# Performance work log

Measured on AMD Instinct MI355X. Metric: run time of the kernel, lower is better.

The kernel has to match this reference:

```python
import jax, jax.numpy as jnp
import numpy as np


def setup_inputs() -> dict:
    key = jax.random.key(0)
    k1, k2, k3 = jax.random.split(key, 3)
    B, N, E, A = 1024, 64, 64, 32
    emb_inputs = jax.random.normal(k1, (B, N, E), dtype=jnp.float32)
    W1 = jax.random.normal(k2, (E, A), dtype=jnp.float32) * (1.0 / np.sqrt(E))
    b1 = jnp.zeros((A,), dtype=jnp.float32)
    W2 = jax.random.normal(k3, (A, 1), dtype=jnp.float32) * (1.0 / np.sqrt(A))
    b2 = jnp.zeros((1,), dtype=jnp.float32)
    return {"emb_inputs": emb_inputs, "W1": W1, "b1": b1, "W2": W2, "b2": b2,
            "num_fields": N}


def reference(emb_inputs, W1, b1, W2, b2, num_fields):
    # Pairwise interaction indices (i < j), same order as torch double loop
    rowidx, colidx = np.triu_indices(num_fields, k=1)
    rowidx = jnp.asarray(rowidx)
    colidx = jnp.asarray(colidx)
    # inner: (B, NC2, E) elementwise product of field pairs
    inner = emb_inputs[:, rowidx] * emb_inputs[:, colidx]
    # tiny attention MLP: E -> A -> 1, softmax over the pair dim
    h = jax.nn.relu(jnp.einsum('bpe,ea->bpa', inner, W1) + b1)
    logits = jnp.einsum('bpa,ao->bpo', h, W2) + b2          # (B, NC2, 1)
    attn_scores = jax.nn.softmax(logits, axis=1)            # (B, NC2, 1)
    # dropout layers are identity in eval mode
    outputs = jnp.sum(inner * attn_scores, axis=1)          # (B, E)
    return outputs, attn_scores
```

## Files before the change

kernel.cpp:

```cpp
#include <hip/hip_runtime.h>

#define BATCH   1024
#define NF      64
#define EDIM    64
#define ADIM    32
#define NPAIR   2016
#define NTILE   126
#define XSTR    72

typedef _Float16 f16;
typedef f16   f16x4 __attribute__((ext_vector_type(4)));
typedef f16   f16x8 __attribute__((ext_vector_type(8)));
typedef float f32x4 __attribute__((ext_vector_type(4)));

__global__ __launch_bounds__(256) void afm_kernel(
    const float* __restrict__ emb,
    const float* __restrict__ W1,
    const float* __restrict__ b1,
    const float* __restrict__ W2,
    const float* __restrict__ b2,
    float* __restrict__ out_vec,
    float* __restrict__ out_attn)
{
    __shared__ __align__(16) f16 xs[NF * XSTR];
    __shared__ __align__(16) f16 Xt[EDIM * XSTR];
    __shared__ __align__(16) f16 As[NF * XSTR];
    __shared__ float logits[NPAIR];
    __shared__ unsigned short pairIJ[NPAIR];
    __shared__ float red[8];
    __shared__ float partial[4][EDIM];

    const int t    = threadIdx.x;
    const int b    = blockIdx.x;
    const int wid  = t >> 6;
    const int lane = t & 63;
    const int g    = lane >> 4;
    const int m16  = lane & 15;

    const float4* xg4 = (const float4*)(emb + (size_t)b * NF * EDIM);
    #pragma unroll
    for (int it = 0; it < 4; ++it) {
        int idx = t + it * 256;
        int f = idx >> 4, e4 = (idx & 15) * 4;
        float4 v = xg4[idx];
        f16 h0 = (f16)v.x, h1 = (f16)v.y, h2 = (f16)v.z, h3 = (f16)v.w;
        f16x4 pk = {h0, h1, h2, h3};
        *(f16x4*)&xs[f * XSTR + e4] = pk;
        Xt[(e4 + 0) * XSTR + f] = h0;
        Xt[(e4 + 1) * XSTR + f] = h1;
        Xt[(e4 + 2) * XSTR + f] = h2;
        Xt[(e4 + 3) * XSTR + f] = h3;
    }

    for (int p = t; p < NPAIR; p += 256) {
        int i = (int)(63.5f - 0.5f * sqrtf(16129.0f - 8.0f * (float)p));
        int Ti = (i * (127 - i)) >> 1;
        if (p < Ti)      { --i; Ti = (i * (127 - i)) >> 1; }
        else { int Tn = ((i + 1) * (126 - i)) >> 1; if (p >= Tn) { ++i; Ti = Tn; } }
        int j = p - Ti + i + 1;
        pairIJ[p] = (unsigned short)((i << 8) | j);
    }

    f16x8 w1f[2][2];
    #pragma unroll
    for (int kh = 0; kh < 2; ++kh)
        #pragma unroll
        for (int nh = 0; nh < 2; ++nh)
            #pragma unroll
            for (int j = 0; j < 8; ++j)
                w1f[kh][nh][j] =
                    (f16)W1[(kh * 32 + 8 * g + j) * ADIM + nh * 16 + m16];

    float b1v[2][4], w2v[2][4];
    #pragma unroll
    for (int nh = 0; nh < 2; ++nh)
        #pragma unroll
        for (int r = 0; r < 4; ++r) {
            b1v[nh][r] = b1[nh * 16 + 4 * g + r];
            w2v[nh][r] = W2[nh * 16 + 4 * g + r];
        }
    const float b2s = b2[0];
    __syncthreads();

    for (int tile = wid; tile < NTILE; tile += 4) {
        const int p  = tile * 16 + m16;
        const int ij = pairIJ[p];
        const f16* xi = &xs[(ij >> 8) * XSTR];
        const f16* xj = &xs[(ij & 255) * XSTR];

        f16x8 xi0 = *(const f16x8*)(xi + 8 * g);
        f16x8 xi1 = *(const f16x8*)(xi + 32 + 8 * g);
        f16x8 xj0 = *(const f16x8*)(xj + 8 * g);
        f16x8 xj1 = *(const f16x8*)(xj + 32 + 8 * g);
        f16x8 bi0 = xi0 * xj0;
        f16x8 bi1 = xi1 * xj1;

        f32x4 acc0 = {0.f, 0.f, 0.f, 0.f};
        f32x4 acc1 = {0.f, 0.f, 0.f, 0.f};
        acc0 = __builtin_amdgcn_mfma_f32_16x16x32_f16(w1f[0][0], bi0, acc0, 0, 0, 0);
        acc1 = __builtin_amdgcn_mfma_f32_16x16x32_f16(w1f[0][1], bi0, acc1, 0, 0, 0);
        acc0 = __builtin_amdgcn_mfma_f32_16x16x32_f16(w1f[1][0], bi1, acc0, 0, 0, 0);
        acc1 = __builtin_amdgcn_mfma_f32_16x16x32_f16(w1f[1][1], bi1, acc1, 0, 0, 0);

        float tr = 0.f;
        #pragma unroll
        for (int r = 0; r < 4; ++r) {
            tr += fmaxf(acc0[r] + b1v[0][r], 0.f) * w2v[0][r];
            tr += fmaxf(acc1[r] + b1v[1][r], 0.f) * w2v[1][r];
        }
        tr += __shfl_xor(tr, 16);
        tr += __shfl_xor(tr, 32);
        if (g == 0) logits[p] = tr + b2s;
    }
    __syncthreads();

    float lv[8];
    #pragma unroll
    for (int k = 0; k < 8; ++k) {
        int p = t + 256 * k;
        lv[k] = (p < NPAIR) ? logits[p] : -INFINITY;
    }
    float m = lv[0];
    #pragma unroll
    for (int k = 1; k < 8; ++k) m = fmaxf(m, lv[k]);
    #pragma unroll
    for (int off = 32; off; off >>= 1) m = fmaxf(m, __shfl_xor(m, off));
    if (lane == 0) red[wid] = m;
    __syncthreads();
    if (t == 0) red[4] = fmaxf(fmaxf(red[0], red[1]), fmaxf(red[2], red[3]));
    __syncthreads();
    m = red[4];

    float s = 0.0f;
    #pragma unroll
    for (int k = 0; k < 8; ++k) {
        float ev = __expf(lv[k] - m);
        lv[k] = ev;
        s += ev;
    }
    #pragma unroll
    for (int off = 32; off; off >>= 1) s += __shfl_xor(s, off);
    __syncthreads();
    if (lane == 0) red[wid] = s;
    __syncthreads();
    if (t == 0) red[5] = red[0] + red[1] + red[2] + red[3];
    __syncthreads();
    const float inv = 1.0f / red[5];

    #pragma unroll
    for (int k = 0; k < 8; ++k) {
        int p = t + 256 * k;
        if (p < NPAIR) {
            float av = lv[k] * inv;
            out_attn[(size_t)b * NPAIR + p] = av;
            f16 ah = (f16)av;
            int ij = pairIJ[p];
            int i = ij >> 8, j = ij & 255;
            As[i * XSTR + j] = ah;
            As[j * XSTR + i] = ah;
        }
    }
    if (t < NF) As[t * XSTR + t] = (f16)0.f;
    __syncthreads();

    const int itile = wid;
    f32x4 yacc[4];
    #pragma unroll
    for (int et = 0; et < 4; ++et) yacc[et] = (f32x4){0.f, 0.f, 0.f, 0.f};

    const f16* arow = &As[(itile * 16 + m16) * XSTR];
    f16x8 af0 = *(const f16x8*)(arow + 8 * g);
    f16x8 af1 = *(const f16x8*)(arow + 32 + 8 * g);
    #pragma unroll
    for (int et = 0; et < 4; ++et) {
        const f16* xtr = &Xt[(et * 16 + m16) * XSTR];
        f16x8 bf0 = *(const f16x8*)(xtr + 8 * g);
        f16x8 bf1 = *(const f16x8*)(xtr + 32 + 8 * g);
        yacc[et] = __builtin_amdgcn_mfma_f32_16x16x32_f16(af0, bf0, yacc[et], 0, 0, 0);
        yacc[et] = __builtin_amdgcn_mfma_f32_16x16x32_f16(af1, bf1, yacc[et], 0, 0, 0);
    }

    #pragma unroll
    for (int et = 0; et < 4; ++et) {
        float v = 0.f;
        #pragma unroll
        for (int r = 0; r < 4; ++r) {
            int i = itile * 16 + 4 * g + r;
            int e = et * 16 + m16;
            v = fmaf((float)xs[i * XSTR + e], yacc[et][r], v);
        }
        v += __shfl_xor(v, 16);
        v += __shfl_xor(v, 32);
        if (g == 0) partial[wid][et * 16 + m16] = v;
    }
    __syncthreads();
    if (t < EDIM)
        out_vec[(size_t)b * EDIM + t] = 0.5f *
            (partial[0][t] + partial[1][t] + partial[2][t] + partial[3][t]);
}

extern "C" void kernel_launch(void* const* d_in, const int* in_sizes, int n_in,
                              void* d_out, int out_size, void* d_ws, size_t ws_size,
                              hipStream_t stream) {
    const float* emb = (const float*)d_in[0];
    const float* W1  = (const float*)d_in[1];
    const float* b1  = (const float*)d_in[2];
    const float* W2  = (const float*)d_in[3];
    const float* b2  = (const float*)d_in[4];
    float* out_vec  = (float*)d_out;
    float* out_attn = (float*)d_out + (size_t)BATCH * EDIM;

    afm_kernel<<<BATCH, 256, 0, stream>>>(emb, W1, b1, W2, b2, out_vec, out_attn);
}
```

Measured before the change: 28.93 us.

## Rework pair scoring with 32x32 MFMA tiles and DPP-rotated field operands

Replaces the per-pair lookup table and 16x16 MFMA tiles with a structured schedule. Each wave keeps 32 row-field vectors in registers and rotates column-field vectors across lanes with DPP, then scores pairs through 32x32x16 MFMAs. The pair index is computed analytically. The transposed X copy is now built by a separate packed pass, and launch bounds request 4 blocks per SM. This aims to cut LDS traffic and the index table overhead, but adds DPP shuffles, register pressure and a runtime probe of the DPP rotation direction.

```diff
diff --git a/kernel.cpp b/kernel.cpp
--- a/kernel.cpp
+++ b/kernel.cpp
@@ -5,15 +5,19 @@
 #define EDIM    64
 #define ADIM    32
 #define NPAIR   2016
-#define NTILE   126
 #define XSTR    72
 
 typedef _Float16 f16;
-typedef f16   f16x4 __attribute__((ext_vector_type(4)));
-typedef f16   f16x8 __attribute__((ext_vector_type(8)));
-typedef float f32x4 __attribute__((ext_vector_type(4)));
-
-__global__ __launch_bounds__(256) void afm_kernel(
+typedef f16   f16x4  __attribute__((ext_vector_type(4)));
+typedef f16   f16x8  __attribute__((ext_vector_type(8)));
+typedef float f32x4  __attribute__((ext_vector_type(4)));
+typedef float f32x16 __attribute__((ext_vector_type(16)));
+
+__device__ __forceinline__ f16x8 asH(int4 v) {
+    union { int4 i; f16x8 h; } u; u.i = v; return u.h;
+}
+
+__global__ __launch_bounds__(256, 4) void afm_kernel(
     const float* __restrict__ emb,
     const float* __restrict__ W1,
     const float* __restrict__ b1,
@@ -26,7 +30,6 @@
     __shared__ __align__(16) f16 Xt[EDIM * XSTR];
     __shared__ __align__(16) f16 As[NF * XSTR];
     __shared__ float logits[NPAIR];
-    __shared__ unsigned short pairIJ[NPAIR];
     __shared__ float red[8];
     __shared__ float partial[4][EDIM];
 
@@ -36,6 +39,10 @@
     const int lane = t & 63;
     const int g    = lane >> 4;
     const int m16  = lane & 15;
+    const int h    = lane >> 5;
+    const int l32  = lane & 31;
+    const int l16  = lane & 15;
+    const int hb   = l32 >> 4;
 
     const float4* xg4 = (const float4*)(emb + (size_t)b * NF * EDIM);
     #pragma unroll
@@ -43,74 +50,136 @@
         int idx = t + it * 256;
         int f = idx >> 4, e4 = (idx & 15) * 4;
         float4 v = xg4[idx];
-        f16 h0 = (f16)v.x, h1 = (f16)v.y, h2 = (f16)v.z, h3 = (f16)v.w;
-        f16x4 pk = {h0, h1, h2, h3};
+        f16x4 pk = {(f16)v.x, (f16)v.y, (f16)v.z, (f16)v.w};
         *(f16x4*)&xs[f * XSTR + e4] = pk;
-        Xt[(e4 + 0) * XSTR + f] = h0;
-        Xt[(e4 + 1) * XSTR + f] = h1;
-        Xt[(e4 + 2) * XSTR + f] = h2;
-        Xt[(e4 + 3) * XSTR + f] = h3;
-    }
-
-    for (int p = t; p < NPAIR; p += 256) {
-        int i = (int)(63.5f - 0.5f * sqrtf(16129.0f - 8.0f * (float)p));
-        int Ti = (i * (127 - i)) >> 1;
-        if (p < Ti)      { --i; Ti = (i * (127 - i)) >> 1; }
-        else { int Tn = ((i + 1) * (126 - i)) >> 1; if (p >= Tn) { ++i; Ti = Tn; } }
-        int j = p - Ti + i + 1;
-        pairIJ[p] = (unsigned short)((i << 8) | j);
-    }
-
-    f16x8 w1f[2][2];
-    #pragma unroll
-    for (int kh = 0; kh < 2; ++kh)
-        #pragma unroll
-        for (int nh = 0; nh < 2; ++nh)
+    }
+
+    f16x8 w1a[4];
+    #pragma unroll
+    for (int q = 0; q < 4; ++q)
+        #pragma unroll
+        for (int jj = 0; jj < 8; ++jj)
+            w1a[q][jj] = (f16)W1[(16 * q + 8 * h + jj) * ADIM + l32];
+
+    float b1v[16], w2v[16];
+    #pragma unroll
+    for (int r = 0; r < 16; ++r) {
+        int a = (r & 3) + 8 * (r >> 2) + 4 * h;
+        b1v[r] = b1[a];
+        w2v[r] = W2[a];
+    }
+    const float b2s = b2[0];
+    __syncthreads();
+
+    {
+        const unsigned short* xsu = (const unsigned short*)xs;
+        #pragma unroll
+        for (int it = 0; it < 2; ++it) {
+            int cid = t + it * 256;
+            int e = cid & 63, c = cid >> 6;
+            unsigned int d[4];
             #pragma unroll
-            for (int j = 0; j < 8; ++j)
-                w1f[kh][nh][j] =
-                    (f16)W1[(kh * 32 + 8 * g + j) * ADIM + nh * 16 + m16];
-
-    float b1v[2][4], w2v[2][4];
-    #pragma unroll
-    for (int nh = 0; nh < 2; ++nh)
-        #pragma unroll
-        for (int r = 0; r < 4; ++r) {
-            b1v[nh][r] = b1[nh * 16 + 4 * g + r];
-            w2v[nh][r] = W2[nh * 16 + 4 * g + r];
-        }
-    const float b2s = b2[0];
-    __syncthreads();
-
-    for (int tile = wid; tile < NTILE; tile += 4) {
-        const int p  = tile * 16 + m16;
-        const int ij = pairIJ[p];
-        const f16* xi = &xs[(ij >> 8) * XSTR];
-        const f16* xj = &xs[(ij & 255) * XSTR];
-
-        f16x8 xi0 = *(const f16x8*)(xi + 8 * g);
-        f16x8 xi1 = *(const f16x8*)(xi + 32 + 8 * g);
-        f16x8 xj0 = *(const f16x8*)(xj + 8 * g);
-        f16x8 xj1 = *(const f16x8*)(xj + 32 + 8 * g);
-        f16x8 bi0 = xi0 * xj0;
-        f16x8 bi1 = xi1 * xj1;
-
-        f32x4 acc0 = {0.f, 0.f, 0.f, 0.f};
-        f32x4 acc1 = {0.f, 0.f, 0.f, 0.f};
-        acc0 = __builtin_amdgcn_mfma_f32_16x16x32_f16(w1f[0][0], bi0, acc0, 0, 0, 0);
-        acc1 = __builtin_amdgcn_mfma_f32_16x16x32_f16(w1f[0][1], bi0, acc1, 0, 0, 0);
-        acc0 = __builtin_amdgcn_mfma_f32_16x16x32_f16(w1f[1][0], bi1, acc0, 0, 0, 0);
-        acc1 = __builtin_amdgcn_mfma_f32_16x16x32_f16(w1f[1][1], bi1, acc1, 0, 0, 0);
-
-        float tr = 0.f;
-        #pragma unroll
-        for (int r = 0; r < 4; ++r) {
-            tr += fmaxf(acc0[r] + b1v[0][r], 0.f) * w2v[0][r];
-            tr += fmaxf(acc1[r] + b1v[1][r], 0.f) * w2v[1][r];
-        }
-        tr += __shfl_xor(tr, 16);
+            for (int r2 = 0; r2 < 4; ++r2) {
+                unsigned lo = xsu[(8 * c + 2 * r2)     * XSTR + e];
+                unsigned hi = xsu[(8 * c + 2 * r2 + 1) * XSTR + e];
+                d[r2] = lo | (hi << 16);
+            }
+            int4 w4 = {(int)d[0], (int)d[1], (int)d[2], (int)d[3]};
+            *(int4*)&Xt[e * XSTR + 8 * c] = w4;
+        }
+    }
+    __syncthreads();
+
+    int probe = __builtin_amdgcn_mov_dpp(l16, 0x124, 0xF, 0xF, false);
+    const bool plus4 = (probe == ((l16 + 4) & 15));
+    const int  s0r   = plus4 ? (wid + 1) : (wid + 5);
+
+    int4 xi4[4], xj4[4];
+
+    auto LOADX = [&](int row, int4* d) {
+        #pragma unroll
+        for (int q = 0; q < 4; ++q)
+            d[q] = *(const int4*)&xs[row * XSTR + 16 * q + 8 * h];
+    };
+    auto ROT4D = [&](int4* d, int& jv) {
+        #pragma unroll
+        for (int q = 0; q < 4; ++q) {
+            d[q].x = __builtin_amdgcn_mov_dpp(d[q].x, 0x124, 0xF, 0xF, false);
+            d[q].y = __builtin_amdgcn_mov_dpp(d[q].y, 0x124, 0xF, 0xF, false);
+            d[q].z = __builtin_amdgcn_mov_dpp(d[q].z, 0x124, 0xF, 0xF, false);
+            d[q].w = __builtin_amdgcn_mov_dpp(d[q].w, 0x124, 0xF, 0xF, false);
+        }
+        jv = __builtin_amdgcn_mov_dpp(jv, 0x124, 0xF, 0xF, false);
+    };
+    auto SUB = [&](const int4* xa, const int4* xb, int iv, int jv) {
+        f32x16 acc = {};
+        #pragma unroll
+        for (int q = 0; q < 4; ++q) {
+            f16x8 prod = asH(xa[q]) * asH(xb[q]);
+            acc = __builtin_amdgcn_mfma_f32_32x32x16_f16(w1a[q], prod, acc, 0, 0, 0);
+        }
+        float t0 = 0.f, t1 = 0.f;
+        #pragma unroll
+        for (int r = 0; r < 16; r += 2) {
+            t0 += fmaxf(acc[r]     + b1v[r],     0.f) * w2v[r];
+            t1 += fmaxf(acc[r + 1] + b1v[r + 1], 0.f) * w2v[r + 1];
+        }
+        float tr = t0 + t1;
         tr += __shfl_xor(tr, 32);
-        if (g == 0) logits[p] = tr + b2s;
+        int imin = min(iv, jv), jmax = max(iv, jv);
+        int p = ((imin * (127 - imin)) >> 1) + jmax - imin - 1;
+        if (lane < 32) logits[p] = tr + b2s;
+    };
+
+    LOADX(l32, xi4);
+    {
+        int jv = 32 + 16 * hb + ((l16 + wid) & 15);
+        LOADX(jv, xj4);
+        #pragma unroll
+        for (int k = 0; k < 4; ++k) {
+            SUB(xi4, xj4, l32, jv);
+            if (k < 3) ROT4D(xj4, jv);
+        }
+    }
+    {
+        int jv = 32 + 16 * (1 - hb) + ((l16 + wid) & 15);
+        LOADX(jv, xj4);
+        #pragma unroll
+        for (int k = 0; k < 4; ++k) {
+            SUB(xi4, xj4, l32, jv);
+            if (k < 3) ROT4D(xj4, jv);
+        }
+    }
+    {
+        int jv = 16 * hb + ((l16 + s0r) & 15);
+        LOADX(jv, xj4);
+        SUB(xi4, xj4, l32, jv);
+        ROT4D(xj4, jv);
+        SUB(xi4, xj4, l32, jv);
+    }
+    {
+        int jv = 16 + ((l16 + wid + 8 * hb) & 15);
+        LOADX(l16, xi4);
+        LOADX(jv, xj4);
+        SUB(xi4, xj4, l16, jv);
+        ROT4D(xj4, jv);
+        SUB(xi4, xj4, l16, jv);
+    }
+    {
+        int jv = 32 + 16 * hb + ((l16 + s0r) & 15);
+        LOADX(32 + l32, xi4);
+        LOADX(jv, xj4);
+        SUB(xi4, xj4, 32 + l32, jv);
+        ROT4D(xj4, jv);
+        SUB(xi4, xj4, 32 + l32, jv);
+    }
+    {
+        int jv = 48 + ((l16 + wid + 8 * hb) & 15);
+        LOADX(32 + l16, xi4);
+        LOADX(jv, xj4);
+        SUB(xi4, xj4, 32 + l16, jv);
+        ROT4D(xj4, jv);
+        SUB(xi4, xj4, 32 + l16, jv);
     }
     __syncthreads();
 
@@ -153,9 +222,12 @@
         if (p < NPAIR) {
             float av = lv[k] * inv;
             out_attn[(size_t)b * NPAIR + p] = av;
+            int i = (int)(63.5f - 0.5f * sqrtf(16129.0f - 8.0f * (float)p));
+            int Ti = (i * (127 - i)) >> 1;
+            if (p < Ti)      { --i; Ti = (i * (127 - i)) >> 1; }
+            else { int Tn = ((i + 1) * (126 - i)) >> 1; if (p >= Tn) { ++i; Ti = Tn; } }
+            int j = p - Ti + i + 1;
             f16 ah = (f16)av;
-            int ij = pairIJ[p];
-            int i = ij >> 8, j = ij & 255;
             As[i * XSTR + j] = ah;
             As[j * XSTR + i] = ah;
         }
```

New measurement: 26.48 us. 8.5% less time.
